# Optimization experiments

Hardware: AMD Instinct MI355X
Metric: run time of the kernel (lower is better)

The kernel has to match this reference:

```python
import jax, jax.numpy as jnp
import numpy as np

B, D, N, L, M = 32, 64, 128, 192, 32  # batch, channels, nodes, seq_len, modes
LH = L // 2 + 1  # rfft length = 97


def setup_inputs() -> dict:
    key = jax.random.key(0)
    k1, k2, k3 = jax.random.split(key, 3)
    scale = 1.0 / (D * D)  # 1/(in_channels*out_channels)
    q = jax.random.normal(k1, (B, D, N, L), dtype=jnp.float32)
    w_real = scale * jax.random.uniform(k2, (N, D, D, M), dtype=jnp.float32)
    w_imag = scale * jax.random.uniform(k3, (N, D, D, M), dtype=jnp.float32)
    return {"q": q, "w_real": w_real, "w_imag": w_imag}


def reference(q, w_real, w_imag):
    # mode_select_method='lowest' -> index = [0, 1, ..., M-1] (static)
    index = np.arange(M)
    x = jnp.transpose(q, (0, 2, 1, 3))            # [B, N, D, L]
    x_ft = jnp.fft.rfft(x, axis=-1)               # [B, N, D, LH] complex64
    w = (w_real + 1j * w_imag).astype(jnp.complex64)  # [N, D, D, M]
    sel = x_ft[..., index]                        # gather selected modes [B, N, D, M]
    # fused replacement of the per-mode einsum loop: one batched complex einsum
    out_sel = jnp.einsum('bnim,niom->bnom', sel, w)  # [B, N, D, M]
    out_ft = jnp.zeros((B, N, D, LH), dtype=jnp.complex64).at[..., :M].set(out_sel)
    out = jnp.fft.irfft(out_ft, n=L, axis=-1)     # [B, N, D, L] real
    return jnp.transpose(out, (0, 2, 1, 3))       # [B, D, N, L]
```

## Files before the change

### kernel.cpp

```cpp
#include <hip/hip_runtime.h>
#include <stdint.h>


typedef __attribute__((ext_vector_type(8))) short short8;
typedef __attribute__((ext_vector_type(4))) float f32x4;
typedef __attribute__((ext_vector_type(4))) unsigned short u16x4;

__device__ __forceinline__ unsigned short f2bf(float f) {
  union { float fv; uint32_t u; } v; v.fv = f;
  uint32_t u = v.u;
  u += 0x7fffu + ((u >> 16) & 1u);
  return (unsigned short)(u >> 16);
}

__device__ __forceinline__ f32x4 zero4() { f32x4 z; z[0]=0.f; z[1]=0.f; z[2]=0.f; z[3]=0.f; return z; }

#define TWO_PI_OVER_L (6.283185307179586f / 192.0f)

__global__ __launch_bounds__(512, 2)
void k1_dft(const float* __restrict__ q, unsigned short* __restrict__ Xp) {
  extern __shared__ char smem[];
  const int t = threadIdx.x, lane = t & 63, w = t >> 6;
  const int n = blockIdx.x >> 1, ih = blockIdx.x & 1;

  unsigned short* qb = (unsigned short*)smem;
  char* Fb = smem + 65536;

  for (int idx = t; idx < 64 * 192; idx += 512) {
    int cat = idx / 192, l = idx - cat * 192;
    int m = cat >> 1;
    int r = (m * l) % 192;
    float ang = (float)r * TWO_PI_OVER_L;
    float v = (cat & 1) ? -__sinf(ang) : __cosf(ang);
    *(unsigned short*)(Fb + cat * 400 + l * 2) = f2bf(v);
  }

  f32x4 acc[8][4];
#pragma unroll
  for (int a = 0; a < 8; ++a)
#pragma unroll
    for (int bq = 0; bq < 4; ++bq) acc[a][bq] = zero4();

  for (int kc = 0; kc < 6; ++kc) {
#pragma unroll
    for (int j = 0; j < 16; ++j) {
      int f = j * 512 + t;
      int lg = f & 7, b = (f >> 3) & 31, il = f >> 8;
      const float4 v = *(const float4*)(q + (((b * 64 + ih * 32 + il) * 128 + n) * 192 + kc * 32 + lg * 4));
      u16x4 h; h[0] = f2bf(v.x); h[1] = f2bf(v.y); h[2] = f2bf(v.z); h[3] = f2bf(v.w);
      *(u16x4*)(qb + (il * 32 + b) * 32 + lg * 4) = h;
    }
    __syncthreads();

    short8 Bf[4];
#pragma unroll
    for (int nt = 0; nt < 4; ++nt) {
      int cat = nt * 16 + (lane & 15);
      Bf[nt] = *(const short8*)(Fb + cat * 400 + (kc * 32 + (lane >> 4) * 8) * 2);
    }
#pragma unroll
    for (int mt = 0; mt < 8; ++mt) {
      int Mt = w * 8 + mt;
      int il = Mt >> 1;
      int b = (Mt & 1) * 16 + (lane & 15);
      short8 A = *(const short8*)((const char*)qb + ((il * 32 + b) * 32 + (lane >> 4) * 8) * 2);
#pragma unroll
      for (int nt = 0; nt < 4; ++nt)
        acc[mt][nt] = __builtin_amdgcn_mfma_f32_16x16x32_bf16(A, Bf[nt], acc[mt][nt], 0, 0, 0);
    }
    __syncthreads();
  }

#pragma unroll
  for (int mt = 0; mt < 8; ++mt) {
    int Mt = w * 8 + mt;
    int il = Mt >> 1;
    int b0 = (Mt & 1) * 16 + (lane >> 4) * 4;
#pragma unroll
    for (int nt = 0; nt < 4; ++nt) {
      int cat = nt * 16 + (lane & 15);
      char* base = smem + cat * 2320 + il * 2;
      f32x4 v = acc[mt][nt];
#pragma unroll
      for (int r = 0; r < 4; ++r)
        *(unsigned short*)(base + (b0 + r) * 72) = f2bf(v[r]);
    }
  }
  __syncthreads();

  const int nbase = n * 131072;
#pragma unroll
  for (int j = 0; j < 16; ++j) {
    int f = j * 512 + t;
    int l2 = f & 63, Mt2 = (f >> 6) & 1, c = (f >> 7) & 1, m = f >> 8;
    int cat = 2 * m + c;
    int b = Mt2 * 16 + (l2 & 15);
    int i0 = (l2 >> 4) * 8;
    const char* base = smem + cat * 2320 + b * 72 + i0 * 2;
    u16x4 lo = *(const u16x4*)(base);
    u16x4 hi = *(const u16x4*)(base + 8);
    short8 vv;
    vv[0] = (short)lo[0]; vv[1] = (short)lo[1]; vv[2] = (short)lo[2]; vv[3] = (short)lo[3];
    vv[4] = (short)hi[0]; vv[5] = (short)hi[1]; vv[6] = (short)hi[2]; vv[7] = (short)hi[3];
    int off = nbase + ((((m * 2 + c) * 2 + ih) * 2 + Mt2) * 64 + l2) * 8;
    *(short8*)(Xp + off) = vv;
  }
}

#define K2_OSTRIDE 34
#define K2_ISTRIDE 546
#define K2_CSTRIDE 34944
__global__ __launch_bounds__(512, 2)
void k2f_mix(const float* __restrict__ wr, const float* __restrict__ wi,
             const unsigned short* __restrict__ Xp, unsigned short* __restrict__ Yp) {
  extern __shared__ char smem[];
  unsigned short* T = (unsigned short*)smem;
  const int t = threadIdx.x, lane = t & 63, w = t >> 6;
  const int n = blockIdx.x >> 2, oq = blockIdx.x & 3;
  const int ol = lane & 15, il0 = (lane >> 4) * 8;

#pragma unroll
  for (int j = 0; j < 32; ++j) {
    int f = j * 512 + t;
    int mg = f & 7, o = (f >> 3) & 15, i = (f >> 7) & 63, c = (f >> 13) & 1;
    const float* src = (c ? wi : wr) + ((n * 64 + i) * 64 + oq * 16 + o) * 32 + mg * 4;
    float4 v = *(const float4*)src;
    u16x4 h; h[0] = f2bf(v.x); h[1] = f2bf(v.y); h[2] = f2bf(v.z); h[3] = f2bf(v.w);
    *(u16x4*)(T + c * K2_CSTRIDE + i * K2_ISTRIDE + o * K2_OSTRIDE + mg * 4) = h;
  }
  __syncthreads();

#pragma unroll
  for (int mm = 0; mm < 4; ++mm) {
    int m = w * 4 + mm;
    f32x4 acc[2][2];
#pragma unroll
    for (int a = 0; a < 2; ++a)
#pragma unroll
      for (int b2 = 0; b2 < 2; ++b2) acc[a][b2] = zero4();

#pragma unroll
    for (int ic = 0; ic < 2; ++ic) {
      const unsigned short* xb = Xp + n * 131072 + m * 4096 + ic * 1024 + lane * 8;
      short8 Ar0 = *(const short8*)(xb);
      short8 Ar1 = *(const short8*)(xb + 512);
      short8 Ai0 = *(const short8*)(xb + 2048);
      short8 Ai1 = *(const short8*)(xb + 2048 + 512);

      const unsigned short* tb = T + (ic * 32 + il0) * K2_ISTRIDE + ol * K2_OSTRIDE + m;
      short8 Br, Bi, nBi;
#pragma unroll
      for (int e = 0; e < 8; ++e) {
        Br[e] = (short)tb[e * K2_ISTRIDE];
        Bi[e] = (short)tb[K2_CSTRIDE + e * K2_ISTRIDE];
        nBi[e] = Bi[e] ^ (short)0x8000;
      }

      acc[0][0] = __builtin_amdgcn_mfma_f32_16x16x32_bf16(Ar0, Br,  acc[0][0], 0, 0, 0);
      acc[0][0] = __builtin_amdgcn_mfma_f32_16x16x32_bf16(Ai0, nBi, acc[0][0], 0, 0, 0);
      acc[0][1] = __builtin_amdgcn_mfma_f32_16x16x32_bf16(Ar1, Br,  acc[0][1], 0, 0, 0);
      acc[0][1] = __builtin_amdgcn_mfma_f32_16x16x32_bf16(Ai1, nBi, acc[0][1], 0, 0, 0);
      acc[1][0] = __builtin_amdgcn_mfma_f32_16x16x32_bf16(Ar0, Bi,  acc[1][0], 0, 0, 0);
      acc[1][0] = __builtin_amdgcn_mfma_f32_16x16x32_bf16(Ai0, Br,  acc[1][0], 0, 0, 0);
      acc[1][1] = __builtin_amdgcn_mfma_f32_16x16x32_bf16(Ar1, Bi,  acc[1][1], 0, 0, 0);
      acc[1][1] = __builtin_amdgcn_mfma_f32_16x16x32_bf16(Ai1, Br,  acc[1][1], 0, 0, 0);
    }

    const int g = lane >> 4;
#pragma unroll
    for (int cc = 0; cc < 2; ++cc) {
      int cat = 2 * m + cc;
#pragma unroll
      for (int Mt = 0; Mt < 2; ++Mt) {
        f32x4 v = acc[cc][Mt];
#pragma unroll
        for (int r = 0; r < 4; ++r) {
          int b = Mt * 16 + g * 4 + r;
          Yp[((n * 32 + b) * 64 + cat) * 64 + oq * 16 + ol] = f2bf(v[r]);
        }
      }
    }
  }
}

__global__ __launch_bounds__(256, 4)
void k3_idft(const unsigned short* __restrict__ Yp, float* __restrict__ out) {
  extern __shared__ char smem[];
  unsigned short* Yl = (unsigned short*)smem;
  float* ol = (float*)(smem + 8192);
  const int t = threadIdx.x, lane = t & 63, w = t >> 6;
  const int n = blockIdx.x & 127, b = blockIdx.x >> 7;

  const unsigned short* ysrc = Yp + (n * 32 + b) * 4096;
#pragma unroll
  for (int j = 0; j < 2; ++j) {
    int f = j * 256 + t;
    *(short8*)(Yl + f * 8) = *(const short8*)(ysrc + f * 8);
  }

  short8 Af[3][2];
#pragma unroll
  for (int jm = 0; jm < 3; ++jm) {
    int Mt = w + 4 * jm;
    int lt = Mt * 16 + (lane & 15);
#pragma unroll
    for (int kc = 0; kc < 2; ++kc) {
#pragma unroll
      for (int e = 0; e < 8; ++e) {
        int cat = kc * 32 + (lane >> 4) * 8 + e;
        int m = cat >> 1;
        int r = (m * lt) % 192;
        float ang = (float)r * TWO_PI_OVER_L;
        float coef = (m == 0) ? (1.0f / 192.0f) : (2.0f / 192.0f);
        float v = ((cat & 1) ? -__sinf(ang) : __cosf(ang)) * coef;
        Af[jm][kc][e] = (short)f2bf(v);
      }
    }
  }
  __syncthreads();

  f32x4 acc[3][4];
#pragma unroll
  for (int a = 0; a < 3; ++a)
#pragma unroll
    for (int bq = 0; bq < 4; ++bq) acc[a][bq] = zero4();

#pragma unroll
  for (int kc = 0; kc < 2; ++kc) {
    short8 Bf[4];
#pragma unroll
    for (int nt = 0; nt < 4; ++nt)
#pragma unroll
      for (int e = 0; e < 8; ++e) {
        int cat = kc * 32 + (lane >> 4) * 8 + e;
        Bf[nt][e] = (short)Yl[cat * 64 + nt * 16 + (lane & 15)];
      }
#pragma unroll
    for (int jm = 0; jm < 3; ++jm)
#pragma unroll
      for (int nt = 0; nt < 4; ++nt)
        acc[jm][nt] = __builtin_amdgcn_mfma_f32_16x16x32_bf16(Af[jm][kc], Bf[nt], acc[jm][nt], 0, 0, 0);
  }

#pragma unroll
  for (int jm = 0; jm < 3; ++jm) {
    int Mt = w + 4 * jm;
    int l0 = Mt * 16 + (lane >> 4) * 4;
#pragma unroll
    for (int nt = 0; nt < 4; ++nt) {
      int o = nt * 16 + (lane & 15);
      int lp = l0 ^ ((o & 7) << 2);
      *(f32x4*)(ol + o * 192 + lp) = acc[jm][nt];
    }
  }
  __syncthreads();

  float* dst = out + (b * 64 * 128 + n) * 192;
#pragma unroll
  for (int j = 0; j < 12; ++j) {
    int f = j * 256 + t;
    int o = f / 48, g = f - o * 48;
    int lp = g * 4;
    int l = lp ^ ((o & 7) << 2);
    f32x4 v = *(const f32x4*)(ol + o * 192 + lp);
    *(f32x4*)(dst + o * (128 * 192) + l) = v;
  }
}

extern "C" void kernel_launch(void* const* d_in, const int* in_sizes, int n_in,
                              void* d_out, int out_size, void* d_ws, size_t ws_size,
                              hipStream_t stream) {
  const float* q  = (const float*)d_in[0];
  const float* wr = (const float*)d_in[1];
  const float* wi = (const float*)d_in[2];
  float* out = (float*)d_out;

  unsigned short* Xp = (unsigned short*)d_ws;
  unsigned short* Yp = Xp + 16777216;

  hipFuncSetAttribute((const void*)k1_dft,  hipFuncAttributeMaxDynamicSharedMemorySize, 148480);
  hipFuncSetAttribute((const void*)k2f_mix, hipFuncAttributeMaxDynamicSharedMemorySize, 139776);
  hipFuncSetAttribute((const void*)k3_idft, hipFuncAttributeMaxDynamicSharedMemorySize, 57344);

  k1_dft<<<dim3(256), dim3(512), 148480, stream>>>(q, Xp);
  k2f_mix<<<dim3(512), dim3(512), 139776, stream>>>(wr, wi, Xp, Yp);
  k3_idft<<<dim3(4096), dim3(256), 57344, stream>>>(Yp, out);
}
```

Measured before the change: 192.0 us.

## Fuse DFT, complex mode mixing and inverse DFT into one kernel

```diff
diff --git a/kernel.cpp b/kernel.cpp
--- a/kernel.cpp
+++ b/kernel.cpp
@@ -17,14 +17,29 @@
 
 #define TWO_PI_OVER_L (6.283185307179586f / 192.0f)
 
+#define QB_RSTR   40
+#define F_CSTR    200
+#define X_CSTR    1176
+#define X_BSTR    72
+#define W_CSTR    36992
+#define W_OSTR    2312
+#define W_MSTR    72
+#define Y_BSTR    1160
+#define Y_OSTR    72
+
 __global__ __launch_bounds__(512, 2)
-void k1_dft(const float* __restrict__ q, unsigned short* __restrict__ Xp) {
+void fb_fused(const float* __restrict__ q, const float* __restrict__ wr,
+              const float* __restrict__ wi, float* __restrict__ out) {
   extern __shared__ char smem[];
+  unsigned short* qb = (unsigned short*)smem;
+  unsigned short* Fb = (unsigned short*)(smem + 81920);
+  unsigned short* X  = (unsigned short*)smem;
+  unsigned short* Wt = (unsigned short*)smem;
+  unsigned short* Yt = (unsigned short*)smem;
+
   const int t = threadIdx.x, lane = t & 63, w = t >> 6;
-  const int n = blockIdx.x >> 1, ih = blockIdx.x & 1;
-
-  unsigned short* qb = (unsigned short*)smem;
-  char* Fb = smem + 65536;
+  const int l15 = lane & 15, g = lane >> 4;
+  const int n = blockIdx.x >> 1, bh = blockIdx.x & 1;
 
   for (int idx = t; idx < 64 * 192; idx += 512) {
     int cat = idx / 192, l = idx - cat * 192;
@@ -32,238 +47,157 @@
     int r = (m * l) % 192;
     float ang = (float)r * TWO_PI_OVER_L;
     float v = (cat & 1) ? -__sinf(ang) : __cosf(ang);
-    *(unsigned short*)(Fb + cat * 400 + l * 2) = f2bf(v);
-  }
-
-  f32x4 acc[8][4];
+    Fb[cat * F_CSTR + l] = f2bf(v);
+  }
+
+  f32x4 acc1[8][4];
 #pragma unroll
   for (int a = 0; a < 8; ++a)
 #pragma unroll
-    for (int bq = 0; bq < 4; ++bq) acc[a][bq] = zero4();
+    for (int bq = 0; bq < 4; ++bq) acc1[a][bq] = zero4();
 
   for (int kc = 0; kc < 6; ++kc) {
 #pragma unroll
     for (int j = 0; j < 16; ++j) {
       int f = j * 512 + t;
-      int lg = f & 7, b = (f >> 3) & 31, il = f >> 8;
-      const float4 v = *(const float4*)(q + (((b * 64 + ih * 32 + il) * 128 + n) * 192 + kc * 32 + lg * 4));
+      int lg = f & 7, b = (f >> 3) & 15, i = f >> 7;
+      const float4 v = *(const float4*)(q + (((bh * 16 + b) * 64 + i) * 128 + n) * 192 + kc * 32 + lg * 4);
       u16x4 h; h[0] = f2bf(v.x); h[1] = f2bf(v.y); h[2] = f2bf(v.z); h[3] = f2bf(v.w);
-      *(u16x4*)(qb + (il * 32 + b) * 32 + lg * 4) = h;
+      *(u16x4*)(qb + (i * 16 + b) * QB_RSTR + lg * 4) = h;
     }
     __syncthreads();
 
     short8 Bf[4];
 #pragma unroll
     for (int nt = 0; nt < 4; ++nt) {
-      int cat = nt * 16 + (lane & 15);
-      Bf[nt] = *(const short8*)(Fb + cat * 400 + (kc * 32 + (lane >> 4) * 8) * 2);
+      int cat = nt * 16 + l15;
+      Bf[nt] = *(const short8*)(Fb + cat * F_CSTR + kc * 32 + g * 8);
     }
 #pragma unroll
     for (int mt = 0; mt < 8; ++mt) {
-      int Mt = w * 8 + mt;
-      int il = Mt >> 1;
-      int b = (Mt & 1) * 16 + (lane & 15);
-      short8 A = *(const short8*)((const char*)qb + ((il * 32 + b) * 32 + (lane >> 4) * 8) * 2);
+      int i = w * 8 + mt;
+      short8 A = *(const short8*)(qb + (i * 16 + l15) * QB_RSTR + g * 8);
 #pragma unroll
       for (int nt = 0; nt < 4; ++nt)
-        acc[mt][nt] = __builtin_amdgcn_mfma_f32_16x16x32_bf16(A, Bf[nt], acc[mt][nt], 0, 0, 0);
+        acc1[mt][nt] = __builtin_amdgcn_mfma_f32_16x16x32_bf16(A, Bf[nt], acc1[mt][nt], 0, 0, 0);
     }
     __syncthreads();
   }
 
 #pragma unroll
   for (int mt = 0; mt < 8; ++mt) {
-    int Mt = w * 8 + mt;
-    int il = Mt >> 1;
-    int b0 = (Mt & 1) * 16 + (lane >> 4) * 4;
+    int i = w * 8 + mt;
 #pragma unroll
     for (int nt = 0; nt < 4; ++nt) {
-      int cat = nt * 16 + (lane & 15);
-      char* base = smem + cat * 2320 + il * 2;
-      f32x4 v = acc[mt][nt];
+      int cat = nt * 16 + l15;
+      f32x4 v = acc1[mt][nt];
 #pragma unroll
       for (int r = 0; r < 4; ++r)
-        *(unsigned short*)(base + (b0 + r) * 72) = f2bf(v[r]);
+        X[cat * X_CSTR + (g * 4 + r) * X_BSTR + i] = f2bf(v[r]);
     }
   }
   __syncthreads();
 
-  const int nbase = n * 131072;
-#pragma unroll
-  for (int j = 0; j < 16; ++j) {
-    int f = j * 512 + t;
-    int l2 = f & 63, Mt2 = (f >> 6) & 1, c = (f >> 7) & 1, m = f >> 8;
-    int cat = 2 * m + c;
-    int b = Mt2 * 16 + (l2 & 15);
-    int i0 = (l2 >> 4) * 8;
-    const char* base = smem + cat * 2320 + b * 72 + i0 * 2;
-    u16x4 lo = *(const u16x4*)(base);
-    u16x4 hi = *(const u16x4*)(base + 8);
-    short8 vv;
-    vv[0] = (short)lo[0]; vv[1] = (short)lo[1]; vv[2] = (short)lo[2]; vv[3] = (short)lo[3];
-    vv[4] = (short)hi[0]; vv[5] = (short)hi[1]; vv[6] = (short)hi[2]; vv[7] = (short)hi[3];
-    int off = nbase + ((((m * 2 + c) * 2 + ih) * 2 + Mt2) * 64 + l2) * 8;
-    *(short8*)(Xp + off) = vv;
-  }
-}
-
-#define K2_OSTRIDE 34
-#define K2_ISTRIDE 546
-#define K2_CSTRIDE 34944
-__global__ __launch_bounds__(512, 2)
-void k2f_mix(const float* __restrict__ wr, const float* __restrict__ wi,
-             const unsigned short* __restrict__ Xp, unsigned short* __restrict__ Yp) {
-  extern __shared__ char smem[];
-  unsigned short* T = (unsigned short*)smem;
-  const int t = threadIdx.x, lane = t & 63, w = t >> 6;
-  const int n = blockIdx.x >> 2, oq = blockIdx.x & 3;
-  const int ol = lane & 15, il0 = (lane >> 4) * 8;
-
-#pragma unroll
-  for (int j = 0; j < 32; ++j) {
-    int f = j * 512 + t;
-    int mg = f & 7, o = (f >> 3) & 15, i = (f >> 7) & 63, c = (f >> 13) & 1;
-    const float* src = (c ? wi : wr) + ((n * 64 + i) * 64 + oq * 16 + o) * 32 + mg * 4;
-    float4 v = *(const float4*)src;
-    u16x4 h; h[0] = f2bf(v.x); h[1] = f2bf(v.y); h[2] = f2bf(v.z); h[3] = f2bf(v.w);
-    *(u16x4*)(T + c * K2_CSTRIDE + i * K2_ISTRIDE + o * K2_OSTRIDE + mg * 4) = h;
-  }
+  short8 Xr[4][2][2];
+#pragma unroll
+  for (int mm = 0; mm < 4; ++mm)
+#pragma unroll
+    for (int cc = 0; cc < 2; ++cc)
+#pragma unroll
+      for (int ic = 0; ic < 2; ++ic) {
+        int cat = w * 8 + mm * 2 + cc;
+        Xr[mm][cc][ic] = *(const short8*)(X + cat * X_CSTR + l15 * X_BSTR + ic * 32 + g * 8);
+      }
   __syncthreads();
 
-#pragma unroll
-  for (int mm = 0; mm < 4; ++mm) {
-    int m = w * 4 + mm;
-    f32x4 acc[2][2];
-#pragma unroll
-    for (int a = 0; a < 2; ++a)
-#pragma unroll
-      for (int b2 = 0; b2 < 2; ++b2) acc[a][b2] = zero4();
-
-#pragma unroll
-    for (int ic = 0; ic < 2; ++ic) {
-      const unsigned short* xb = Xp + n * 131072 + m * 4096 + ic * 1024 + lane * 8;
-      short8 Ar0 = *(const short8*)(xb);
-      short8 Ar1 = *(const short8*)(xb + 512);
-      short8 Ai0 = *(const short8*)(xb + 2048);
-      short8 Ai1 = *(const short8*)(xb + 2048 + 512);
-
-      const unsigned short* tb = T + (ic * 32 + il0) * K2_ISTRIDE + ol * K2_OSTRIDE + m;
-      short8 Br, Bi, nBi;
+  short8 Af[12][2];
+#pragma unroll
+  for (int Mt = 0; Mt < 12; ++Mt) {
+    int lt = Mt * 16 + l15;
+#pragma unroll
+    for (int kc = 0; kc < 2; ++kc) {
 #pragma unroll
       for (int e = 0; e < 8; ++e) {
-        Br[e] = (short)tb[e * K2_ISTRIDE];
-        Bi[e] = (short)tb[K2_CSTRIDE + e * K2_ISTRIDE];
-        nBi[e] = Bi[e] ^ (short)0x8000;
-      }
-
-      acc[0][0] = __builtin_amdgcn_mfma_f32_16x16x32_bf16(Ar0, Br,  acc[0][0], 0, 0, 0);
-      acc[0][0] = __builtin_amdgcn_mfma_f32_16x16x32_bf16(Ai0, nBi, acc[0][0], 0, 0, 0);
-      acc[0][1] = __builtin_amdgcn_mfma_f32_16x16x32_bf16(Ar1, Br,  acc[0][1], 0, 0, 0);
-      acc[0][1] = __builtin_amdgcn_mfma_f32_16x16x32_bf16(Ai1, nBi, acc[0][1], 0, 0, 0);
-      acc[1][0] = __builtin_amdgcn_mfma_f32_16x16x32_bf16(Ar0, Bi,  acc[1][0], 0, 0, 0);
-      acc[1][0] = __builtin_amdgcn_mfma_f32_16x16x32_bf16(Ai0, Br,  acc[1][0], 0, 0, 0);
-      acc[1][1] = __builtin_amdgcn_mfma_f32_16x16x32_bf16(Ar1, Bi,  acc[1][1], 0, 0, 0);
-      acc[1][1] = __builtin_amdgcn_mfma_f32_16x16x32_bf16(Ai1, Br,  acc[1][1], 0, 0, 0);
-    }
-
-    const int g = lane >> 4;
-#pragma unroll
-    for (int cc = 0; cc < 2; ++cc) {
-      int cat = 2 * m + cc;
-#pragma unroll
-      for (int Mt = 0; Mt < 2; ++Mt) {
-        f32x4 v = acc[cc][Mt];
-#pragma unroll
-        for (int r = 0; r < 4; ++r) {
-          int b = Mt * 16 + g * 4 + r;
-          Yp[((n * 32 + b) * 64 + cat) * 64 + oq * 16 + ol] = f2bf(v[r]);
-        }
-      }
-    }
-  }
-}
-
-__global__ __launch_bounds__(256, 4)
-void k3_idft(const unsigned short* __restrict__ Yp, float* __restrict__ out) {
-  extern __shared__ char smem[];
-  unsigned short* Yl = (unsigned short*)smem;
-  float* ol = (float*)(smem + 8192);
-  const int t = threadIdx.x, lane = t & 63, w = t >> 6;
-  const int n = blockIdx.x & 127, b = blockIdx.x >> 7;
-
-  const unsigned short* ysrc = Yp + (n * 32 + b) * 4096;
-#pragma unroll
-  for (int j = 0; j < 2; ++j) {
-    int f = j * 256 + t;
-    *(short8*)(Yl + f * 8) = *(const short8*)(ysrc + f * 8);
-  }
-
-  short8 Af[3][2];
-#pragma unroll
-  for (int jm = 0; jm < 3; ++jm) {
-    int Mt = w + 4 * jm;
-    int lt = Mt * 16 + (lane & 15);
-#pragma unroll
-    for (int kc = 0; kc < 2; ++kc) {
-#pragma unroll
-      for (int e = 0; e < 8; ++e) {
-        int cat = kc * 32 + (lane >> 4) * 8 + e;
+        int cat = kc * 32 + g * 8 + e;
         int m = cat >> 1;
         int r = (m * lt) % 192;
         float ang = (float)r * TWO_PI_OVER_L;
         float coef = (m == 0) ? (1.0f / 192.0f) : (2.0f / 192.0f);
         float v = ((cat & 1) ? -__sinf(ang) : __cosf(ang)) * coef;
-        Af[jm][kc][e] = (short)f2bf(v);
-      }
-    }
-  }
-  __syncthreads();
-
-  f32x4 acc[3][4];
-#pragma unroll
-  for (int a = 0; a < 3; ++a)
-#pragma unroll
-    for (int bq = 0; bq < 4; ++bq) acc[a][bq] = zero4();
-
-#pragma unroll
-  for (int kc = 0; kc < 2; ++kc) {
-    short8 Bf[4];
-#pragma unroll
-    for (int nt = 0; nt < 4; ++nt)
-#pragma unroll
-      for (int e = 0; e < 8; ++e) {
-        int cat = kc * 32 + (lane >> 4) * 8 + e;
-        Bf[nt][e] = (short)Yl[cat * 64 + nt * 16 + (lane & 15)];
-      }
-#pragma unroll
-    for (int jm = 0; jm < 3; ++jm)
-#pragma unroll
-      for (int nt = 0; nt < 4; ++nt)
-        acc[jm][nt] = __builtin_amdgcn_mfma_f32_16x16x32_bf16(Af[jm][kc], Bf[nt], acc[jm][nt], 0, 0, 0);
-  }
-
-#pragma unroll
-  for (int jm = 0; jm < 3; ++jm) {
-    int Mt = w + 4 * jm;
-    int l0 = Mt * 16 + (lane >> 4) * 4;
-#pragma unroll
-    for (int nt = 0; nt < 4; ++nt) {
-      int o = nt * 16 + (lane & 15);
-      int lp = l0 ^ ((o & 7) << 2);
-      *(f32x4*)(ol + o * 192 + lp) = acc[jm][nt];
-    }
-  }
-  __syncthreads();
-
-  float* dst = out + (b * 64 * 128 + n) * 192;
-#pragma unroll
-  for (int j = 0; j < 12; ++j) {
-    int f = j * 256 + t;
-    int o = f / 48, g = f - o * 48;
-    int lp = g * 4;
-    int l = lp ^ ((o & 7) << 2);
-    f32x4 v = *(const f32x4*)(ol + o * 192 + lp);
-    *(f32x4*)(dst + o * (128 * 192) + l) = v;
+        Af[Mt][kc][e] = (short)f2bf(v);
+      }
+    }
+  }
+
+  for (int oq = 0; oq < 4; ++oq) {
+#pragma unroll
+    for (int j = 0; j < 32; ++j) {
+      int f = j * 512 + t;
+      int mg = f & 7, o = (f >> 3) & 15, i = (f >> 7) & 63, c = (f >> 13) & 1;
+      const float* src = (c ? wi : wr) + ((n * 64 + i) * 64 + oq * 16 + o) * 32 + mg * 4;
+      float4 v = *(const float4*)src;
+      unsigned short* d = Wt + c * W_CSTR + o * W_OSTR + (mg * 4) * W_MSTR + i;
+      d[0]          = f2bf(v.x);
+      d[W_MSTR]     = f2bf(v.y);
+      d[2 * W_MSTR] = f2bf(v.z);
+      d[3 * W_MSTR] = f2bf(v.w);
+    }
+    __syncthreads();
+
+    f32x4 accY[4][2];
+#pragma unroll
+    for (int a = 0; a < 4; ++a)
+#pragma unroll
+      for (int c2 = 0; c2 < 2; ++c2) accY[a][c2] = zero4();
+
+#pragma unroll
+    for (int mm = 0; mm < 4; ++mm) {
+      int m = w * 4 + mm;
+#pragma unroll
+      for (int ic = 0; ic < 2; ++ic) {
+        const unsigned short* wb = Wt + l15 * W_OSTR + m * W_MSTR + ic * 32 + g * 8;
+        short8 Br = *(const short8*)(wb);
+        short8 Bi = *(const short8*)(wb + W_CSTR);
+        short8 nBi;
+#pragma unroll
+        for (int e = 0; e < 8; ++e) nBi[e] = Bi[e] ^ (short)0x8000;
+        accY[mm][0] = __builtin_amdgcn_mfma_f32_16x16x32_bf16(Xr[mm][0][ic], Br,  accY[mm][0], 0, 0, 0);
+        accY[mm][0] = __builtin_amdgcn_mfma_f32_16x16x32_bf16(Xr[mm][1][ic], nBi, accY[mm][0], 0, 0, 0);
+        accY[mm][1] = __builtin_amdgcn_mfma_f32_16x16x32_bf16(Xr[mm][0][ic], Bi,  accY[mm][1], 0, 0, 0);
+        accY[mm][1] = __builtin_amdgcn_mfma_f32_16x16x32_bf16(Xr[mm][1][ic], Br,  accY[mm][1], 0, 0, 0);
+      }
+    }
+    __syncthreads();
+
+#pragma unroll
+    for (int mm = 0; mm < 4; ++mm)
+#pragma unroll
+      for (int cc = 0; cc < 2; ++cc) {
+        int cat = (w * 4 + mm) * 2 + cc;
+        f32x4 v = accY[mm][cc];
+#pragma unroll
+        for (int r = 0; r < 4; ++r)
+          Yt[(g * 4 + r) * Y_BSTR + l15 * Y_OSTR + cat] = f2bf(v[r]);
+      }
+    __syncthreads();
+
+#pragma unroll
+    for (int bb = 0; bb < 2; ++bb) {
+      int b = w * 2 + bb;
+      short8 Bf2[2];
+#pragma unroll
+      for (int kc = 0; kc < 2; ++kc)
+        Bf2[kc] = *(const short8*)(Yt + b * Y_BSTR + l15 * Y_OSTR + kc * 32 + g * 8);
+      float* dst = out + (((bh * 16 + b) * 64 + oq * 16 + l15) * 128 + n) * 192;
+#pragma unroll
+      for (int Mt = 0; Mt < 12; ++Mt) {
+        f32x4 acc = zero4();
+        acc = __builtin_amdgcn_mfma_f32_16x16x32_bf16(Af[Mt][0], Bf2[0], acc, 0, 0, 0);
+        acc = __builtin_amdgcn_mfma_f32_16x16x32_bf16(Af[Mt][1], Bf2[1], acc, 0, 0, 0);
+        *(f32x4*)(dst + Mt * 16 + g * 4) = acc;
+      }
+    }
+    __syncthreads();
   }
 }
 
@@ -275,14 +209,6 @@
   const float* wi = (const float*)d_in[2];
   float* out = (float*)d_out;
 
-  unsigned short* Xp = (unsigned short*)d_ws;
-  unsigned short* Yp = Xp + 16777216;
-
-  hipFuncSetAttribute((const void*)k1_dft,  hipFuncAttributeMaxDynamicSharedMemorySize, 148480);
-  hipFuncSetAttribute((const void*)k2f_mix, hipFuncAttributeMaxDynamicSharedMemorySize, 139776);
-  hipFuncSetAttribute((const void*)k3_idft, hipFuncAttributeMaxDynamicSharedMemorySize, 57344);
-
-  k1_dft<<<dim3(256), dim3(512), 148480, stream>>>(q, Xp);
-  k2f_mix<<<dim3(512), dim3(512), 139776, stream>>>(wr, wi, Xp, Yp);
-  k3_idft<<<dim3(4096), dim3(256), 57344, stream>>>(Yp, out);
+  hipFuncSetAttribute((const void*)fb_fused, hipFuncAttributeMaxDynamicSharedMemorySize, 150528);
+  fb_fused<<<dim3(256), dim3(512), 150528, stream>>>(q, wr, wi, out);
 }
```

After: 236.7 us. 1.23x slower.

## Restructure forward DFT kernel to read contiguous q rows per batch group

Applied to the files above, without the earlier changes.

```diff
diff --git a/kernel.cpp b/kernel.cpp
--- a/kernel.cpp
+++ b/kernel.cpp
@@ -17,14 +17,17 @@
 
 #define TWO_PI_OVER_L (6.283185307179586f / 192.0f)
 
-__global__ __launch_bounds__(512, 2)
-void k1_dft(const float* __restrict__ q, unsigned short* __restrict__ Xp) {
+__global__ __launch_bounds__(512, 1)
+void k1n_dft(const float* __restrict__ q, unsigned short* __restrict__ Xp) {
   extern __shared__ char smem[];
+  float* qS = (float*)smem;
+  unsigned short* Fb = (unsigned short*)(smem + 100352);
+  unsigned short* XE = (unsigned short*)(smem + 125952);
   const int t = threadIdx.x, lane = t & 63, w = t >> 6;
-  const int n = blockIdx.x >> 1, ih = blockIdx.x & 1;
-
-  unsigned short* qb = (unsigned short*)smem;
-  char* Fb = smem + 65536;
+  const int l15 = lane & 15, g = lane >> 4;
+  const int bid = blockIdx.x;
+  const int ih = bid & 1, bq = (bid >> 1) & 7, nq = bid >> 4;
+  const int b0 = bq * 4;
 
   for (int idx = t; idx < 64 * 192; idx += 512) {
     int cat = idx / 192, l = idx - cat * 192;
@@ -32,78 +35,73 @@
     int r = (m * l) % 192;
     float ang = (float)r * TWO_PI_OVER_L;
     float v = (cat & 1) ? -__sinf(ang) : __cosf(ang);
-    *(unsigned short*)(Fb + cat * 400 + l * 2) = f2bf(v);
-  }
-
-  f32x4 acc[8][4];
-#pragma unroll
-  for (int a = 0; a < 8; ++a)
-#pragma unroll
-    for (int bq = 0; bq < 4; ++bq) acc[a][bq] = zero4();
-
-  for (int kc = 0; kc < 6; ++kc) {
-#pragma unroll
-    for (int j = 0; j < 16; ++j) {
-      int f = j * 512 + t;
-      int lg = f & 7, b = (f >> 3) & 31, il = f >> 8;
-      const float4 v = *(const float4*)(q + (((b * 64 + ih * 32 + il) * 128 + n) * 192 + kc * 32 + lg * 4));
-      u16x4 h; h[0] = f2bf(v.x); h[1] = f2bf(v.y); h[2] = f2bf(v.z); h[3] = f2bf(v.w);
-      *(u16x4*)(qb + (il * 32 + b) * 32 + lg * 4) = h;
+    Fb[cat * 200 + l] = f2bf(v);
+  }
+
+  for (int nn = 0; nn < 4; ++nn) {
+    const int n = nq * 4 + nn;
+
+    float4 stg[12];
+#pragma unroll
+    for (int j = 0; j < 12; ++j) {
+      int fq = (w * 12 + j) * 64 + lane;
+      int row = fq / 48;
+      int qd = fq - row * 48;
+      int b = b0 + (row >> 5);
+      int i = ih * 32 + (row & 31);
+      stg[j] = *(const float4*)(q + ((size_t)((b * 64 + i) * 128 + n)) * 192 + qd * 4);
+    }
+#pragma unroll
+    for (int j = 0; j < 12; ++j) {
+      int fq = (w * 12 + j) * 64 + lane;
+      int row = fq / 48;
+      int qd = fq - row * 48;
+      *(float4*)(qS + row * 196 + qd * 4) = stg[j];
     }
     __syncthreads();
 
-    short8 Bf[4];
+    f32x4 acc[4];
+#pragma unroll
+    for (int a = 0; a < 4; ++a) acc[a] = zero4();
+
+    const int row = w * 16 + l15;
+#pragma unroll
+    for (int kc = 0; kc < 6; ++kc) {
+      f32x4 lo = *(const f32x4*)(qS + row * 196 + kc * 32 + g * 8);
+      f32x4 hi = *(const f32x4*)(qS + row * 196 + kc * 32 + g * 8 + 4);
+      short8 A;
+      A[0] = (short)f2bf(lo[0]); A[1] = (short)f2bf(lo[1]);
+      A[2] = (short)f2bf(lo[2]); A[3] = (short)f2bf(lo[3]);
+      A[4] = (short)f2bf(hi[0]); A[5] = (short)f2bf(hi[1]);
+      A[6] = (short)f2bf(hi[2]); A[7] = (short)f2bf(hi[3]);
+#pragma unroll
+      for (int nt = 0; nt < 4; ++nt) {
+        short8 Bf = *(const short8*)(Fb + (nt * 16 + l15) * 200 + kc * 32 + g * 8);
+        acc[nt] = __builtin_amdgcn_mfma_f32_16x16x32_bf16(A, Bf, acc[nt], 0, 0, 0);
+      }
+    }
+
+    const int b_loc = w >> 1, i_base = (w & 1) * 16 + g * 4;
 #pragma unroll
     for (int nt = 0; nt < 4; ++nt) {
-      int cat = nt * 16 + (lane & 15);
-      Bf[nt] = *(const short8*)(Fb + cat * 400 + (kc * 32 + (lane >> 4) * 8) * 2);
-    }
-#pragma unroll
-    for (int mt = 0; mt < 8; ++mt) {
-      int Mt = w * 8 + mt;
-      int il = Mt >> 1;
-      int b = (Mt & 1) * 16 + (lane & 15);
-      short8 A = *(const short8*)((const char*)qb + ((il * 32 + b) * 32 + (lane >> 4) * 8) * 2);
-#pragma unroll
-      for (int nt = 0; nt < 4; ++nt)
-        acc[mt][nt] = __builtin_amdgcn_mfma_f32_16x16x32_bf16(A, Bf[nt], acc[mt][nt], 0, 0, 0);
+      int cat = nt * 16 + l15;
+      f32x4 v = acc[nt];
+#pragma unroll
+      for (int r = 0; r < 4; ++r)
+        XE[cat * 128 + b_loc * 32 + i_base + r] = f2bf(v[r]);
     }
     __syncthreads();
-  }
-
-#pragma unroll
-  for (int mt = 0; mt < 8; ++mt) {
-    int Mt = w * 8 + mt;
-    int il = Mt >> 1;
-    int b0 = (Mt & 1) * 16 + (lane >> 4) * 4;
-#pragma unroll
-    for (int nt = 0; nt < 4; ++nt) {
-      int cat = nt * 16 + (lane & 15);
-      char* base = smem + cat * 2320 + il * 2;
-      f32x4 v = acc[mt][nt];
-#pragma unroll
-      for (int r = 0; r < 4; ++r)
-        *(unsigned short*)(base + (b0 + r) * 72) = f2bf(v[r]);
-    }
-  }
-  __syncthreads();
-
-  const int nbase = n * 131072;
-#pragma unroll
-  for (int j = 0; j < 16; ++j) {
-    int f = j * 512 + t;
-    int l2 = f & 63, Mt2 = (f >> 6) & 1, c = (f >> 7) & 1, m = f >> 8;
-    int cat = 2 * m + c;
-    int b = Mt2 * 16 + (l2 & 15);
-    int i0 = (l2 >> 4) * 8;
-    const char* base = smem + cat * 2320 + b * 72 + i0 * 2;
-    u16x4 lo = *(const u16x4*)(base);
-    u16x4 hi = *(const u16x4*)(base + 8);
-    short8 vv;
-    vv[0] = (short)lo[0]; vv[1] = (short)lo[1]; vv[2] = (short)lo[2]; vv[3] = (short)lo[3];
-    vv[4] = (short)hi[0]; vv[5] = (short)hi[1]; vv[6] = (short)hi[2]; vv[7] = (short)hi[3];
-    int off = nbase + ((((m * 2 + c) * 2 + ih) * 2 + Mt2) * 64 + l2) * 8;
-    *(short8*)(Xp + off) = vv;
+
+#pragma unroll
+    for (int cc2 = 0; cc2 < 2; ++cc2) {
+      int ch = cc2 * 512 + t;
+      int m = ch >> 5, c = (ch >> 4) & 1, g2 = (ch >> 2) & 3, dl = ch & 3;
+      short8 v = *(const short8*)(XE + (2 * m + c) * 128 + dl * 32 + g2 * 8);
+      int lanep = g2 * 16 + (b0 & 15) + dl;
+      int off = n * 131072 + ((((m * 2 + c) * 2 + ih) * 2 + (b0 >> 4)) * 64 + lanep) * 8;
+      *(short8*)(Xp + off) = v;
+    }
+    __syncthreads();
   }
 }
 
@@ -259,8 +257,8 @@
 #pragma unroll
   for (int j = 0; j < 12; ++j) {
     int f = j * 256 + t;
-    int o = f / 48, g = f - o * 48;
-    int lp = g * 4;
+    int o = f / 48, g2 = f - o * 48;
+    int lp = g2 * 4;
     int l = lp ^ ((o & 7) << 2);
     f32x4 v = *(const f32x4*)(ol + o * 192 + lp);
     *(f32x4*)(dst + o * (128 * 192) + l) = v;
@@ -278,11 +276,11 @@
   unsigned short* Xp = (unsigned short*)d_ws;
   unsigned short* Yp = Xp + 16777216;
 
-  hipFuncSetAttribute((const void*)k1_dft,  hipFuncAttributeMaxDynamicSharedMemorySize, 148480);
+  hipFuncSetAttribute((const void*)k1n_dft, hipFuncAttributeMaxDynamicSharedMemorySize, 142336);
   hipFuncSetAttribute((const void*)k2f_mix, hipFuncAttributeMaxDynamicSharedMemorySize, 139776);
   hipFuncSetAttribute((const void*)k3_idft, hipFuncAttributeMaxDynamicSharedMemorySize, 57344);
 
-  k1_dft<<<dim3(256), dim3(512), 148480, stream>>>(q, Xp);
+  k1n_dft<<<dim3(512), dim3(512), 142336, stream>>>(q, Xp);
   k2f_mix<<<dim3(512), dim3(512), 139776, stream>>>(wr, wi, Xp, Yp);
   k3_idft<<<dim3(4096), dim3(256), 57344, stream>>>(Yp, out);
 }
```

After: 193.1 us. Within noise of the previous version (+0.6%).
